# Kernel tuning notes

Hardware: AMD Instinct MI355X
Metric: run time of the kernel (lower is better)

The kernel has to match this reference:

```python
import jax, jax.numpy as jnp
import numpy as np

E = 8        # num_experts
TOP_K = 2    # num_experts_per_tok
AUX_COEFF = 0.01


def _grok_ffn(x, g, u, d):
    # down(gelu(gate(x)) * up(x)); torch F.gelu default is exact (erf)
    return (jax.nn.gelu(x @ g.T, approximate=False) * (x @ u.T)) @ d.T


def setup_inputs() -> dict:
    key = jax.random.key(0)
    ks = jax.random.split(key, 8)
    B, T, D, H = 4, 4096, 1024, 2816
    s = 0.02
    return {
        "x": jax.random.normal(ks[0], (B, T, D), dtype=jnp.float32),
        "gate_w": jax.random.normal(ks[1], (E, D), dtype=jnp.float32) * 0.01,
        "wg": jax.random.normal(ks[2], (E, H, D), dtype=jnp.float32) * s,
        "wu": jax.random.normal(ks[3], (E, H, D), dtype=jnp.float32) * s,
        "wd": jax.random.normal(ks[4], (E, D, H), dtype=jnp.float32) * s,
        "sg": jax.random.normal(ks[5], (H, D), dtype=jnp.float32) * s,
        "su": jax.random.normal(ks[6], (H, D), dtype=jnp.float32) * s,
        "sd": jax.random.normal(ks[7], (D, H), dtype=jnp.float32) * s,
    }


def reference(x, gate_w, wg, wu, wd, sg, su, sd):
    B, T, D = x.shape
    xf = x.reshape(B * T, D)  # (N, D)

    # ---- router ----
    logits = (xf @ gate_w.T).astype(jnp.float32)          # (N, E)
    top_v, top_i = jax.lax.top_k(logits, TOP_K)           # (N, K)
    expert_weights = jax.nn.softmax(top_v, axis=-1)       # (N, K)
    gates = jax.nn.softmax(logits, axis=-1)               # (N, E)
    f = jax.nn.one_hot(top_i[:, 0], E, dtype=jnp.float32).mean(axis=0)
    P = gates.mean(axis=0)
    aux_loss = AUX_COEFF * E * (f * P).sum()

    # combine weight per (token, expert): sum_k w[t,k] * [idx[t,k]==e]
    onehot = jax.nn.one_hot(top_i, E, dtype=jnp.float32)  # (N, K, E)
    combine = (expert_weights[..., None] * onehot).sum(axis=1)  # (N, E)

    # ---- expert compute (loop over small fixed expert count) ----
    out = jnp.zeros_like(xf)
    for e in range(E):
        out = out + combine[:, e:e + 1] * _grok_ffn(xf, wg[e], wu[e], wd[e])

    out = out.reshape(B, T, D)
    out = out + _grok_ffn(x, sg, su, sd)  # shared expert
    return out, aux_loss
```

## Files before the change

kernel.cpp:

```cpp
#include <hip/hip_runtime.h>
#include <cstdint>

#define NE 8
#define NEX 9
#define NTOK 16384
#define DDIM 1024
#define HDIM 2816

typedef unsigned short u16;
typedef __attribute__((ext_vector_type(8))) short short8;
typedef __attribute__((ext_vector_type(4))) float f32x4;

__device__ __forceinline__ u16 f2bf(float f) {
  uint32_t u = __builtin_bit_cast(uint32_t, f);
  u += 0x7FFFu + ((u >> 16) & 1u);
  return (u16)(u >> 16);
}

__device__ __forceinline__ float wave_reduce_sum(float v) {
  for (int off = 32; off > 0; off >>= 1) v += __shfl_xor(v, off, 64);
  return v;
}

#define GLOAD16(gsrc, ldst)                                                   \
  __builtin_amdgcn_global_load_lds(                                           \
      (const __attribute__((address_space(1))) unsigned int*)(gsrc),          \
      (__attribute__((address_space(3))) unsigned int*)(ldst), 16, 0, 0)

__device__ __forceinline__ void xcd_map(int NT, int MT, int* nt, int* mt) {
  int lin = blockIdx.y * NT + blockIdx.x;
  int nwg = NT * MT;
  int q = nwg >> 3, r = nwg & 7;
  int xcd = lin & 7, idx = lin >> 3;
  int nl = (xcd < r) ? (xcd * (q + 1) + idx) : (r * (q + 1) + (xcd - r) * q + idx);
  *nt = nl / MT;
  *mt = nl % MT;
}

__global__ void init_kernel(int* cnt, float* Pacc, float* fcnt) {
  int t = threadIdx.x;
  if (t < NEX) cnt[t] = (t == 8) ? NTOK : 0;
  if (t < NE) { Pacc[t] = 0.f; fcnt[t] = 0.f; }
}

struct CvtArgs {
  const float* src[7];
  u16* dst[7];
  long long cum[8];
};

__global__ void convert_kernel(CvtArgs a) {
  long long stride = (long long)gridDim.x * blockDim.x;
  long long total = a.cum[7];
  for (long long g = (long long)blockIdx.x * blockDim.x + threadIdx.x; g < total; g += stride) {
    int s = 0;
    while (g >= a.cum[s + 1]) s++;
    long long off = (g - a.cum[s]) * 4;
    float4 v = *reinterpret_cast<const float4*>(a.src[s] + off);
    union { u16 u[4]; uint2 w; } o;
    o.u[0] = f2bf(v.x); o.u[1] = f2bf(v.y); o.u[2] = f2bf(v.z); o.u[3] = f2bf(v.w);
    *reinterpret_cast<uint2*>(a.dst[s] + off) = o.w;
  }
}

__global__ __launch_bounds__(256) void router_kernel(
    const float* __restrict__ x, const float* __restrict__ gw,
    int* __restrict__ tok, float* __restrict__ wtl,
    int* __restrict__ cnt, float* __restrict__ Pacc, float* __restrict__ fcnt) {
  int lane = threadIdx.x & 63;
  int wv = threadIdx.x >> 6;
  __shared__ float red[4][16];
  float pP[NE], pF[NE];
#pragma unroll
  for (int e = 0; e < NE; e++) { pP[e] = 0.f; pF[e] = 0.f; }
  int t0 = blockIdx.x * 16 + wv * 4;
  for (int ti = 0; ti < 4; ti++) {
    int t = t0 + ti;
    float part[NE];
#pragma unroll
    for (int e = 0; e < NE; e++) part[e] = 0.f;
    const float* xp = x + (size_t)t * DDIM;
#pragma unroll
    for (int j = 0; j < 16; j++) {
      float xv = xp[lane + j * 64];
#pragma unroll
      for (int e = 0; e < NE; e++) part[e] += xv * gw[e * DDIM + lane + j * 64];
    }
#pragma unroll
    for (int e = 0; e < NE; e++) part[e] = wave_reduce_sum(part[e]);
    if (lane == 0) {
      float v0 = -1e30f, v1 = -1e30f; int i0 = 0, i1 = 0;
#pragma unroll
      for (int e = 0; e < NE; e++) {
        float v = part[e];
        if (v > v0) { v1 = v0; i1 = i0; v0 = v; i0 = e; }
        else if (v > v1) { v1 = v; i1 = e; }
      }
      float e1 = expf(v1 - v0);
      float w0 = 1.f / (1.f + e1);
      float w1 = e1 * w0;
      float s = 0.f, g[NE];
#pragma unroll
      for (int e = 0; e < NE; e++) { g[e] = expf(part[e] - v0); s += g[e]; }
      float inv = 1.f / s;
#pragma unroll
      for (int e = 0; e < NE; e++) pP[e] += g[e] * inv;
      pF[i0] += 1.f;
      int p0 = atomicAdd(&cnt[i0], 1);
      tok[i0 * NTOK + p0] = t; wtl[i0 * NTOK + p0] = w0;
      int p1 = atomicAdd(&cnt[i1], 1);
      tok[i1 * NTOK + p1] = t; wtl[i1 * NTOK + p1] = w1;
      tok[8 * NTOK + t] = t; wtl[8 * NTOK + t] = 1.f;
    }
  }
  if (lane == 0) {
#pragma unroll
    for (int e = 0; e < NE; e++) { red[wv][e] = pP[e]; red[wv][e + 8] = pF[e]; }
  }
  __syncthreads();
  if (threadIdx.x < 16) {
    float s = red[0][threadIdx.x] + red[1][threadIdx.x] + red[2][threadIdx.x] + red[3][threadIdx.x];
    if (threadIdx.x < 8) atomicAdd(&Pacc[threadIdx.x], s);
    else atomicAdd(&fcnt[threadIdx.x - 8], s);
  }
}

__global__ void finalize_router(const int* cnt, int* offs, const float* Pacc,
                                const float* fcnt, float* out_aux) {
  if (threadIdx.x == 0 && blockIdx.x == 0) {
    int p = NTOK;
    for (int e = 0; e < NE; e++) { offs[e] = p; p += cnt[e]; }
    offs[8] = 0;
    float aux = 0.f;
    for (int e = 0; e < NE; e++)
      aux += (fcnt[e] * (1.f / NTOK)) * (Pacc[e] * (1.f / NTOK));
    *out_aux = 0.01f * 8.f * aux;
  }
}


template<bool WB>
__global__ __launch_bounds__(256, 2) void pass1_kernel(
    const u16* __restrict__ xbf, const void* __restrict__ WGall,
    const void* __restrict__ WUall, const void* __restrict__ SG,
    const void* __restrict__ SU, const int* __restrict__ tok,
    const int* __restrict__ cnt, const int* __restrict__ offs,
    u16* __restrict__ Abuf, int e0, int ab_off) {
  int nt, mt;
  xcd_map(gridDim.x, gridDim.y, &nt, &mt);
  int e = e0 + blockIdx.z;
  int Me = cnt[e];
  if (mt * 128 >= Me) return;
  int base = offs[e];
  int ab = (ab_off < 0) ? base : ab_off;

  __shared__ u16 lX[128 * 64];
  __shared__ u16 lG[128 * 64];
  __shared__ u16 lU[128 * 64];

  int tid = threadIdx.x, lane = tid & 63, wv = tid >> 6;
  int wr = wv >> 1, wc = wv & 1;
  size_t wst = (size_t)HDIM * DDIM;
  int swsrc = ((lane & 7) ^ (lane >> 3)) * 8;

  const u16* gx[4];
#pragma unroll
  for (int q = 0; q < 4; q++) {
    int r = (wv * 4 + q) * 8 + (lane >> 3);
    int gm = mt * 128 + r;
    int tk = (gm < Me) ? tok[e * NTOK + gm] : 0;
    gx[q] = xbf + (size_t)tk * DDIM + swsrc;
  }

  const u16 *gg[4], *gu[4];
  const float *pg0 = nullptr, *pu0 = nullptr;
  int st_r0 = 0, st_chunk = 0, st_win = 0;
  if constexpr (WB) {
    const u16* G = (e == 8) ? (const u16*)SG : (const u16*)WGall + (size_t)e * wst;
    const u16* U = (e == 8) ? (const u16*)SU : (const u16*)WUall + (size_t)e * wst;
#pragma unroll
    for (int q = 0; q < 4; q++) {
      int r = (wv * 4 + q) * 8 + (lane >> 3);
      gg[q] = G + (size_t)(nt * 128 + r) * DDIM + swsrc;
      gu[q] = U + (size_t)(nt * 128 + r) * DDIM + swsrc;
    }
  } else {
    const float* G = (e == 8) ? (const float*)SG : (const float*)WGall + (size_t)e * wst;
    const float* U = (e == 8) ? (const float*)SU : (const float*)WUall + (size_t)e * wst;
    st_r0 = wv * 32 + (lane >> 4);
    int c0 = (lane & 15) * 4;
    st_chunk = c0 >> 3; st_win = c0 & 7;
    pg0 = G + (size_t)(nt * 128 + st_r0) * DDIM + c0;
    pu0 = U + (size_t)(nt * 128 + st_r0) * DDIM + c0;
  }

  f32x4 accG[4][4] = {};
  f32x4 accU[4][4] = {};

  for (int kt = 0; kt < DDIM / 64; kt++) {
    __syncthreads();
    int ko = kt * 64;
#pragma unroll
    for (int q = 0; q < 4; q++)
      GLOAD16(gx[q] + ko, lX + (wv * 4 + q) * 512);
    if constexpr (WB) {
#pragma unroll
      for (int q = 0; q < 4; q++) {
        int ldsoff = (wv * 4 + q) * 512;
        GLOAD16(gg[q] + ko, lG + ldsoff);
        GLOAD16(gu[q] + ko, lU + ldsoff);
      }
    } else {
#pragma unroll
      for (int q = 0; q < 8; q++) {
        int row = st_r0 + q * 4;
        int pc = (((st_chunk ^ (row & 7)) << 3) | st_win);
        float4 vg = *reinterpret_cast<const float4*>(pg0 + ko + q * 4 * DDIM);
        float4 vu = *reinterpret_cast<const float4*>(pu0 + ko + q * 4 * DDIM);
        union { u16 h[4]; uint2 w; } og, ou;
        og.h[0] = f2bf(vg.x); og.h[1] = f2bf(vg.y); og.h[2] = f2bf(vg.z); og.h[3] = f2bf(vg.w);
        ou.h[0] = f2bf(vu.x); ou.h[1] = f2bf(vu.y); ou.h[2] = f2bf(vu.z); ou.h[3] = f2bf(vu.w);
        *reinterpret_cast<uint2*>(lG + row * 64 + pc) = og.w;
        *reinterpret_cast<uint2*>(lU + row * 64 + pc) = ou.w;
      }
    }
    asm volatile("s_waitcnt vmcnt(0)" ::: "memory");
    __syncthreads();

    __builtin_amdgcn_s_setprio(1);
#pragma unroll
    for (int kk = 0; kk < 2; kk++) {
      int kbs = (((kk * 4 + (lane >> 4)) ^ (lane & 7))) * 8;
      short8 af[4];
#pragma unroll
      for (int m = 0; m < 4; m++) {
        int row = wr * 64 + m * 16 + (lane & 15);
        af[m] = *reinterpret_cast<const short8*>(lX + row * 64 + kbs);
      }
#pragma unroll
      for (int n = 0; n < 4; n++) {
        int hr = wc * 64 + n * 16 + (lane & 15);
        short8 bg = *reinterpret_cast<const short8*>(lG + hr * 64 + kbs);
        short8 bu = *reinterpret_cast<const short8*>(lU + hr * 64 + kbs);
#pragma unroll
        for (int m = 0; m < 4; m++) {
          accG[m][n] = __builtin_amdgcn_mfma_f32_16x16x32_bf16(af[m], bg, accG[m][n], 0, 0, 0);
          accU[m][n] = __builtin_amdgcn_mfma_f32_16x16x32_bf16(af[m], bu, accU[m][n], 0, 0, 0);
        }
      }
    }
    __builtin_amdgcn_s_setprio(0);
  }

  int rsub = (lane >> 4) * 4, csub = lane & 15;
#pragma unroll
  for (int m = 0; m < 4; m++) {
#pragma unroll
    for (int i = 0; i < 4; i++) {
      int row = wr * 64 + m * 16 + rsub + i;
      int gm = mt * 128 + row;
      if (gm < Me) {
        size_t rb = (size_t)(base + gm - ab) * HDIM + nt * 128;
#pragma unroll
        for (int n = 0; n < 4; n++) {
          float hg = accG[m][n][i];
          float hu = accU[m][n][i];
          float a = 0.5f * hg * (1.f + erff(hg * 0.70710678118f)) * hu;
          Abuf[rb + wc * 64 + n * 16 + csub] = f2bf(a);
        }
      }
    }
  }
}

template<bool WB>
__global__ __launch_bounds__(256, 2) void pass2_kernel(
    const u16* __restrict__ Abuf, const void* __restrict__ WDall,
    const void* __restrict__ SD, const int* __restrict__ tok,
    const float* __restrict__ wtl, const int* __restrict__ cnt,
    const int* __restrict__ offs, float* __restrict__ out, int e0, int ab_off) {
  int nt, mt;
  xcd_map(gridDim.x, gridDim.y, &nt, &mt);
  int e = e0 + blockIdx.z;
  int Me = cnt[e];
  if (mt * 128 >= Me) return;
  int base = offs[e];
  int ab = (ab_off < 0) ? base : ab_off;
  size_t wst = (size_t)HDIM * DDIM;

  __shared__ u16 lA[128 * 64];
  __shared__ u16 lB[128 * 64];

  int tid = threadIdx.x, lane = tid & 63, wv = tid >> 6;
  int wr = wv >> 1, wc = wv & 1;
  int swsrc = ((lane & 7) ^ (lane >> 3)) * 8;

  const u16* ga[4];
#pragma unroll
  for (int q = 0; q < 4; q++) {
    int r = (wv * 4 + q) * 8 + (lane >> 3);
    int slot = base + mt * 128 + r - ab;
    ga[q] = Abuf + (size_t)slot * HDIM + swsrc;
  }

  const u16* gb[4];
  const float* pd0 = nullptr;
  int st_r0 = 0, st_chunk = 0, st_win = 0;
  if constexpr (WB) {
    const u16* D = (e == 8) ? (const u16*)SD : (const u16*)WDall + (size_t)e * wst;
#pragma unroll
    for (int q = 0; q < 4; q++) {
      int r = (wv * 4 + q) * 8 + (lane >> 3);
      gb[q] = D + (size_t)(nt * 128 + r) * HDIM + swsrc;
    }
  } else {
    const float* D = (e == 8) ? (const float*)SD : (const float*)WDall + (size_t)e * wst;
    st_r0 = wv * 32 + (lane >> 4);
    int c0 = (lane & 15) * 4;
    st_chunk = c0 >> 3; st_win = c0 & 7;
    pd0 = D + (size_t)(nt * 128 + st_r0) * HDIM + c0;
  }

  f32x4 acc[4][4] = {};

  for (int kt = 0; kt < HDIM / 64; kt++) {
    __syncthreads();
    int ko = kt * 64;
#pragma unroll
    for (int q = 0; q < 4; q++)
      GLOAD16(ga[q] + ko, lA + (wv * 4 + q) * 512);
    if constexpr (WB) {
#pragma unroll
      for (int q = 0; q < 4; q++)
        GLOAD16(gb[q] + ko, lB + (wv * 4 + q) * 512);
    } else {
#pragma unroll
      for (int q = 0; q < 8; q++) {
        int row = st_r0 + q * 4;
        int pc = (((st_chunk ^ (row & 7)) << 3) | st_win);
        float4 vd = *reinterpret_cast<const float4*>(pd0 + ko + q * 4 * HDIM);
        union { u16 h[4]; uint2 w; } od;
        od.h[0] = f2bf(vd.x); od.h[1] = f2bf(vd.y); od.h[2] = f2bf(vd.z); od.h[3] = f2bf(vd.w);
        *reinterpret_cast<uint2*>(lB + row * 64 + pc) = od.w;
      }
    }
    asm volatile("s_waitcnt vmcnt(0)" ::: "memory");
    __syncthreads();

    __builtin_amdgcn_s_setprio(1);
#pragma unroll
    for (int kk = 0; kk < 2; kk++) {
      int kbs = (((kk * 4 + (lane >> 4)) ^ (lane & 7))) * 8;
      short8 af[4];
#pragma unroll
      for (int m = 0; m < 4; m++) {
        int row = wr * 64 + m * 16 + (lane & 15);
        af[m] = *reinterpret_cast<const short8*>(lA + row * 64 + kbs);
      }
#pragma unroll
      for (int n = 0; n < 4; n++) {
        int dr = wc * 64 + n * 16 + (lane & 15);
        short8 bd = *reinterpret_cast<const short8*>(lB + dr * 64 + kbs);
#pragma unroll
        for (int m = 0; m < 4; m++)
          acc[m][n] = __builtin_amdgcn_mfma_f32_16x16x32_bf16(af[m], bd, acc[m][n], 0, 0, 0);
      }
    }
    __builtin_amdgcn_s_setprio(0);
  }

  int rsub = (lane >> 4) * 4, csub = lane & 15;
#pragma unroll
  for (int m = 0; m < 4; m++) {
#pragma unroll
    for (int i = 0; i < 4; i++) {
      int row = wr * 64 + m * 16 + rsub + i;
      int gm = mt * 128 + row;
      if (gm < Me) {
        int t = tok[e * NTOK + gm];
        float w = (e == 8) ? 1.f : wtl[e * NTOK + gm];
        size_t ob = (size_t)t * DDIM + nt * 128;
#pragma unroll
        for (int n = 0; n < 4; n++) {
          float v = w * acc[m][n][i];
          int c = wc * 64 + n * 16 + csub;
          if (e == 8) out[ob + c] = v;
          else atomicAdd(&out[ob + c], v);
        }
      }
    }
  }
}

extern "C" void kernel_launch(void* const* d_in, const int* in_sizes, int n_in,
                              void* d_out, int out_size, void* d_ws, size_t ws_size,
                              hipStream_t stream) {
  const float* x  = (const float*)d_in[0];
  const float* gw = (const float*)d_in[1];
  const float* wg = (const float*)d_in[2];
  const float* wu = (const float*)d_in[3];
  const float* wd = (const float*)d_in[4];
  const float* sg = (const float*)d_in[5];
  const float* su = (const float*)d_in[6];
  const float* sd = (const float*)d_in[7];
  float* out = (float*)d_out;

  bool tierG = ws_size >= 379000000ULL;
  bool tierF = !tierG && ws_size >= 327000000ULL;
  bool tierE = !tierG && !tierF && ws_size >= 223000000ULL;
  bool split = tierG || tierF || tierE;
  bool w1cvt = tierG || tierF;
  bool w2cvt = tierG;

  char* ws = (char*)d_ws;
  size_t o = 0;
  auto alloc = [&](size_t bytes) -> void* {
    void* p = ws + o;
    o = (o + bytes + 255) & ~(size_t)255;
    return p;
  };
  u16* xbf = (u16*)alloc((size_t)NTOK * DDIM * 2);
  u16 *wgbf = nullptr, *wubf = nullptr, *sgbf = nullptr, *subf = nullptr;
  u16 *wdbf = nullptr, *sdbf = nullptr;
  if (w1cvt) {
    wgbf = (u16*)alloc((size_t)NE * HDIM * DDIM * 2);
    wubf = (u16*)alloc((size_t)NE * HDIM * DDIM * 2);
    sgbf = (u16*)alloc((size_t)HDIM * DDIM * 2);
    subf = (u16*)alloc((size_t)HDIM * DDIM * 2);
  }
  if (w2cvt) {
    wdbf = (u16*)alloc((size_t)NE * DDIM * HDIM * 2);
    sdbf = (u16*)alloc((size_t)DDIM * HDIM * 2);
  }
  size_t abuf_rows = split ? ((size_t)2 * NTOK + 128) : ((size_t)NTOK + 128);
  u16* Abuf = (u16*)alloc(abuf_rows * HDIM * 2);
  int*   tok  = (int*)alloc((size_t)NEX * NTOK * 4);
  float* wtl  = (float*)alloc((size_t)NEX * NTOK * 4);
  int*   cnt  = (int*)alloc(64);
  int*   offs = (int*)alloc(64);
  float* Pacc = (float*)alloc(64);
  float* fcnt = (float*)alloc(64);

  init_kernel<<<1, 64, 0, stream>>>(cnt, Pacc, fcnt);

  {
    CvtArgs ca;
    long long sizes4[7];
    int nsrc = 0;
    ca.src[nsrc] = x; ca.dst[nsrc] = xbf; sizes4[nsrc] = (long long)NTOK * DDIM / 4; nsrc++;
    if (w1cvt) {
      ca.src[nsrc] = wg; ca.dst[nsrc] = wgbf; sizes4[nsrc] = (long long)NE * HDIM * DDIM / 4; nsrc++;
      ca.src[nsrc] = wu; ca.dst[nsrc] = wubf; sizes4[nsrc] = (long long)NE * HDIM * DDIM / 4; nsrc++;
      ca.src[nsrc] = sg; ca.dst[nsrc] = sgbf; sizes4[nsrc] = (long long)HDIM * DDIM / 4; nsrc++;
      ca.src[nsrc] = su; ca.dst[nsrc] = subf; sizes4[nsrc] = (long long)HDIM * DDIM / 4; nsrc++;
    }
    if (w2cvt) {
      ca.src[nsrc] = wd; ca.dst[nsrc] = wdbf; sizes4[nsrc] = (long long)NE * DDIM * HDIM / 4; nsrc++;
      ca.src[nsrc] = sd; ca.dst[nsrc] = sdbf; sizes4[nsrc] = (long long)DDIM * HDIM / 4; nsrc++;
    }
    ca.cum[0] = 0;
    for (int i = 0; i < 7; i++)
      ca.cum[i + 1] = ca.cum[i] + (i < nsrc ? sizes4[i] : 0);
    convert_kernel<<<4096, 256, 0, stream>>>(ca);
  }

  router_kernel<<<NTOK / 16, 256, 0, stream>>>(x, gw, tok, wtl, cnt, Pacc, fcnt);
  finalize_router<<<1, 64, 0, stream>>>(cnt, offs, Pacc, fcnt, out + (out_size - 1));

  const void *WG, *WU, *SG, *SU, *WD, *SD;
  if (w1cvt) { WG = wgbf; WU = wubf; SG = sgbf; SU = subf; }
  else       { WG = wg;   WU = wu;   SG = sg;   SU = su;   }
  if (w2cvt) { WD = wdbf; SD = sdbf; }
  else       { WD = wd;   SD = sd;   }

  if (split) {
    if (w1cvt) {
      pass1_kernel<true><<<dim3(HDIM / 128, NTOK / 128, 1), 256, 0, stream>>>(
          xbf, WG, WU, SG, SU, tok, cnt, offs, Abuf, 8, 0);
    } else {
      pass1_kernel<false><<<dim3(HDIM / 128, NTOK / 128, 1), 256, 0, stream>>>(
          xbf, WG, WU, SG, SU, tok, cnt, offs, Abuf, 8, 0);
    }
    if (w2cvt) {
      pass2_kernel<true><<<dim3(DDIM / 128, NTOK / 128, 1), 256, 0, stream>>>(
          Abuf, WD, SD, tok, wtl, cnt, offs, out, 8, 0);
    } else {
      pass2_kernel<false><<<dim3(DDIM / 128, NTOK / 128, 1), 256, 0, stream>>>(
          Abuf, WD, SD, tok, wtl, cnt, offs, out, 8, 0);
    }
    if (w1cvt) {
      pass1_kernel<true><<<dim3(HDIM / 128, NTOK / 128, NE), 256, 0, stream>>>(
          xbf, WG, WU, SG, SU, tok, cnt, offs, Abuf, 0, NTOK);
    } else {
      pass1_kernel<false><<<dim3(HDIM / 128, NTOK / 128, NE), 256, 0, stream>>>(
          xbf, WG, WU, SG, SU, tok, cnt, offs, Abuf, 0, NTOK);
    }
    if (w2cvt) {
      pass2_kernel<true><<<dim3(DDIM / 128, NTOK / 128, NE), 256, 0, stream>>>(
          Abuf, WD, SD, tok, wtl, cnt, offs, out, 0, NTOK);
    } else {
      pass2_kernel<false><<<dim3(DDIM / 128, NTOK / 128, NE), 256, 0, stream>>>(
          Abuf, WD, SD, tok, wtl, cnt, offs, out, 0, NTOK);
    }
  } else {
    for (int k = 0; k < NEX; k++) {
      int e = (k == 0) ? 8 : (k - 1);
      pass1_kernel<false><<<dim3(HDIM / 128, NTOK / 128, 1), 256, 0, stream>>>(
          xbf, WG, WU, SG, SU, tok, cnt, offs, Abuf, e, -1);
      pass2_kernel<false><<<dim3(DDIM / 128, NTOK / 128, 1), 256, 0, stream>>>(
          Abuf, WD, SD, tok, wtl, cnt, offs, out, e, -1);
    }
  }
}
```

Baseline: 2.067 ms.

## Alias down-proj bf16 weights onto gate buffer to fit full conversion in less workspace

Merges the two largest workspace tiers into one. Once the routed pass1 has finished with the bf16 gate/up weights, the down-projection weights are converted into that same region, so both GEMM passes can use bf16 weights with less scratch memory. To allow this ordering, the shared expert now runs after the routed experts. The output is therefore zeroed with a memset, and the shared expert adds its result instead of overwriting it. This costs an extra memset and a read-modify-write of the output, and it makes the weight conversion a serial step between the passes.

```diff
diff --git a/kernel.cpp b/kernel.cpp
--- a/kernel.cpp
+++ b/kernel.cpp
@@ -384,7 +384,7 @@
         for (int n = 0; n < 4; n++) {
           float v = w * acc[m][n][i];
           int c = wc * 64 + n * 16 + csub;
-          if (e == 8) out[ob + c] = v;
+          if (e == 8) out[ob + c] = out[ob + c] + v;
           else atomicAdd(&out[ob + c], v);
         }
       }
@@ -405,12 +405,8 @@
   const float* sd = (const float*)d_in[7];
   float* out = (float*)d_out;
 
-  bool tierG = ws_size >= 379000000ULL;
-  bool tierF = !tierG && ws_size >= 327000000ULL;
-  bool tierE = !tierG && !tierF && ws_size >= 223000000ULL;
-  bool split = tierG || tierF || tierE;
-  bool w1cvt = tierG || tierF;
-  bool w2cvt = tierG;
+  bool tierF = ws_size >= 327000000ULL;
+  bool tierE = !tierF && ws_size >= 223000000ULL;
 
   char* ws = (char*)d_ws;
   size_t o = 0;
@@ -422,17 +418,15 @@
   u16* xbf = (u16*)alloc((size_t)NTOK * DDIM * 2);
   u16 *wgbf = nullptr, *wubf = nullptr, *sgbf = nullptr, *subf = nullptr;
   u16 *wdbf = nullptr, *sdbf = nullptr;
-  if (w1cvt) {
+  if (tierF) {
     wgbf = (u16*)alloc((size_t)NE * HDIM * DDIM * 2);
     wubf = (u16*)alloc((size_t)NE * HDIM * DDIM * 2);
     sgbf = (u16*)alloc((size_t)HDIM * DDIM * 2);
     subf = (u16*)alloc((size_t)HDIM * DDIM * 2);
-  }
-  if (w2cvt) {
-    wdbf = (u16*)alloc((size_t)NE * DDIM * HDIM * 2);
-    sdbf = (u16*)alloc((size_t)DDIM * HDIM * 2);
-  }
-  size_t abuf_rows = split ? ((size_t)2 * NTOK + 128) : ((size_t)NTOK + 128);
+    wdbf = wgbf;
+    sdbf = wgbf + (size_t)NE * DDIM * HDIM;
+  }
+  size_t abuf_rows = (tierF || tierE) ? ((size_t)2 * NTOK + 128) : ((size_t)NTOK + 128);
   u16* Abuf = (u16*)alloc(abuf_rows * HDIM * 2);
   int*   tok  = (int*)alloc((size_t)NEX * NTOK * 4);
   float* wtl  = (float*)alloc((size_t)NEX * NTOK * 4);
@@ -441,6 +435,7 @@
   float* Pacc = (float*)alloc(64);
   float* fcnt = (float*)alloc(64);
 
+  hipMemsetAsync(d_out, 0, (size_t)out_size * 4, stream);
   init_kernel<<<1, 64, 0, stream>>>(cnt, Pacc, fcnt);
 
   {
@@ -448,16 +443,12 @@
     long long sizes4[7];
     int nsrc = 0;
     ca.src[nsrc] = x; ca.dst[nsrc] = xbf; sizes4[nsrc] = (long long)NTOK * DDIM / 4; nsrc++;
-    if (w1cvt) {
+    if (tierF) {
       ca.src[nsrc] = wg; ca.dst[nsrc] = wgbf; sizes4[nsrc] = (long long)NE * HDIM * DDIM / 4; nsrc++;
       ca.src[nsrc] = wu; ca.dst[nsrc] = wubf; sizes4[nsrc] = (long long)NE * HDIM * DDIM / 4; nsrc++;
       ca.src[nsrc] = sg; ca.dst[nsrc] = sgbf; sizes4[nsrc] = (long long)HDIM * DDIM / 4; nsrc++;
       ca.src[nsrc] = su; ca.dst[nsrc] = subf; sizes4[nsrc] = (long long)HDIM * DDIM / 4; nsrc++;
     }
-    if (w2cvt) {
-      ca.src[nsrc] = wd; ca.dst[nsrc] = wdbf; sizes4[nsrc] = (long long)NE * DDIM * HDIM / 4; nsrc++;
-      ca.src[nsrc] = sd; ca.dst[nsrc] = sdbf; sizes4[nsrc] = (long long)DDIM * HDIM / 4; nsrc++;
-    }
     ca.cum[0] = 0;
     for (int i = 0; i < 7; i++)
       ca.cum[i + 1] = ca.cum[i] + (i < nsrc ? sizes4[i] : 0);
@@ -467,48 +458,41 @@
   router_kernel<<<NTOK / 16, 256, 0, stream>>>(x, gw, tok, wtl, cnt, Pacc, fcnt);
   finalize_router<<<1, 64, 0, stream>>>(cnt, offs, Pacc, fcnt, out + (out_size - 1));
 
-  const void *WG, *WU, *SG, *SU, *WD, *SD;
-  if (w1cvt) { WG = wgbf; WU = wubf; SG = sgbf; SU = subf; }
-  else       { WG = wg;   WU = wu;   SG = sg;   SU = su;   }
-  if (w2cvt) { WD = wdbf; SD = sdbf; }
-  else       { WD = wd;   SD = sd;   }
-
-  if (split) {
-    if (w1cvt) {
-      pass1_kernel<true><<<dim3(HDIM / 128, NTOK / 128, 1), 256, 0, stream>>>(
-          xbf, WG, WU, SG, SU, tok, cnt, offs, Abuf, 8, 0);
-    } else {
-      pass1_kernel<false><<<dim3(HDIM / 128, NTOK / 128, 1), 256, 0, stream>>>(
-          xbf, WG, WU, SG, SU, tok, cnt, offs, Abuf, 8, 0);
-    }
-    if (w2cvt) {
-      pass2_kernel<true><<<dim3(DDIM / 128, NTOK / 128, 1), 256, 0, stream>>>(
-          Abuf, WD, SD, tok, wtl, cnt, offs, out, 8, 0);
-    } else {
-      pass2_kernel<false><<<dim3(DDIM / 128, NTOK / 128, 1), 256, 0, stream>>>(
-          Abuf, WD, SD, tok, wtl, cnt, offs, out, 8, 0);
-    }
-    if (w1cvt) {
-      pass1_kernel<true><<<dim3(HDIM / 128, NTOK / 128, NE), 256, 0, stream>>>(
-          xbf, WG, WU, SG, SU, tok, cnt, offs, Abuf, 0, NTOK);
-    } else {
-      pass1_kernel<false><<<dim3(HDIM / 128, NTOK / 128, NE), 256, 0, stream>>>(
-          xbf, WG, WU, SG, SU, tok, cnt, offs, Abuf, 0, NTOK);
-    }
-    if (w2cvt) {
-      pass2_kernel<true><<<dim3(DDIM / 128, NTOK / 128, NE), 256, 0, stream>>>(
-          Abuf, WD, SD, tok, wtl, cnt, offs, out, 0, NTOK);
-    } else {
-      pass2_kernel<false><<<dim3(DDIM / 128, NTOK / 128, NE), 256, 0, stream>>>(
-          Abuf, WD, SD, tok, wtl, cnt, offs, out, 0, NTOK);
-    }
+  if (tierF) {
+    pass1_kernel<true><<<dim3(HDIM / 128, NTOK / 128, NE), 256, 0, stream>>>(
+        xbf, wgbf, wubf, sgbf, subf, tok, cnt, offs, Abuf, 0, NTOK);
+    {
+      CvtArgs ca;
+      ca.src[0] = wd; ca.dst[0] = wdbf;
+      ca.src[1] = sd; ca.dst[1] = sdbf;
+      long long s0 = (long long)NE * DDIM * HDIM / 4;
+      long long s1 = (long long)DDIM * HDIM / 4;
+      ca.cum[0] = 0; ca.cum[1] = s0; ca.cum[2] = s0 + s1;
+      for (int i = 3; i <= 7; i++) ca.cum[i] = ca.cum[2];
+      convert_kernel<<<4096, 256, 0, stream>>>(ca);
+    }
+    pass2_kernel<true><<<dim3(DDIM / 128, NTOK / 128, NE), 256, 0, stream>>>(
+        Abuf, wdbf, sdbf, tok, wtl, cnt, offs, out, 0, NTOK);
+    pass1_kernel<true><<<dim3(HDIM / 128, NTOK / 128, 1), 256, 0, stream>>>(
+        xbf, wgbf, wubf, sgbf, subf, tok, cnt, offs, Abuf, 8, 0);
+    pass2_kernel<true><<<dim3(DDIM / 128, NTOK / 128, 1), 256, 0, stream>>>(
+        Abuf, wdbf, sdbf, tok, wtl, cnt, offs, out, 8, 0);
+  } else if (tierE) {
+    pass1_kernel<false><<<dim3(HDIM / 128, NTOK / 128, 1), 256, 0, stream>>>(
+        xbf, wg, wu, sg, su, tok, cnt, offs, Abuf, 8, 0);
+    pass2_kernel<false><<<dim3(DDIM / 128, NTOK / 128, 1), 256, 0, stream>>>(
+        Abuf, wd, sd, tok, wtl, cnt, offs, out, 8, 0);
+    pass1_kernel<false><<<dim3(HDIM / 128, NTOK / 128, NE), 256, 0, stream>>>(
+        xbf, wg, wu, sg, su, tok, cnt, offs, Abuf, 0, NTOK);
+    pass2_kernel<false><<<dim3(DDIM / 128, NTOK / 128, NE), 256, 0, stream>>>(
+        Abuf, wd, sd, tok, wtl, cnt, offs, out, 0, NTOK);
   } else {
     for (int k = 0; k < NEX; k++) {
       int e = (k == 0) ? 8 : (k - 1);
       pass1_kernel<false><<<dim3(HDIM / 128, NTOK / 128, 1), 256, 0, stream>>>(
-          xbf, WG, WU, SG, SU, tok, cnt, offs, Abuf, e, -1);
+          xbf, wg, wu, sg, su, tok, cnt, offs, Abuf, e, -1);
       pass2_kernel<false><<<dim3(DDIM / 128, NTOK / 128, 1), 256, 0, stream>>>(
-          Abuf, WD, SD, tok, wtl, cnt, offs, out, e, -1);
-    }
-  }
-}
+          Abuf, wd, sd, tok, wtl, cnt, offs, out, e, -1);
+    }
+  }
+}
```

Measured after the change: 1.687 ms. 1.22x faster.
